# Performance work log

Measured on AMD Instinct MI355X. Metric: run time of the kernel, lower is better.

The kernel has to match this reference:

```python
import jax, jax.numpy as jnp
import numpy as np

B, N, C = 8, 4096, 512

def setup_inputs() -> dict:
    key = jax.random.key(0)
    k1, k2, k3, k4, k5, k6 = jax.random.split(key, 6)
    x = jax.random.normal(k1, (B, N, C), dtype=jnp.float32)
    adj = jax.random.uniform(k2, (B, C, C), dtype=jnp.float32)
    # params: stored [in, out] so y = x @ W + b (equivalent to torch Linear)
    s = 1.0 / np.sqrt(C)
    Wqkv = jax.random.uniform(k3, (C, 3 * C), dtype=jnp.float32, minval=-s, maxval=s)
    bqkv = jax.random.uniform(k4, (3 * C,), dtype=jnp.float32, minval=-s, maxval=s)
    Wo = jax.random.uniform(k5, (C, C), dtype=jnp.float32, minval=-s, maxval=s)
    bo = jax.random.uniform(k6, (C,), dtype=jnp.float32, minval=-s, maxval=s)
    return {"x": x, "adj": adj, "Wqkv": Wqkv, "bqkv": bqkv, "Wo": Wo, "bo": bo}

def reference(x, adj, Wqkv, bqkv, Wo, bo):
    # qkv projection + ReLU gating
    qkv = jnp.einsum('bnc,cd->bnd', x, Wqkv) + bqkv          # [B,N,3C]
    q, k, v = jnp.split(qkv, 3, axis=-1)                      # each [B,N,C]
    q, k, v = jax.nn.relu(q), jax.nn.relu(k), jax.nn.relu(v)
    dk = q.shape[-1]
    # channel-wise scores: q^T k over tokens -> [B,C,C]
    scores = jnp.einsum('bnc,bnd->bcd', q, k) / jnp.sqrt(jnp.float32(dk))
    attn = jax.nn.softmax(scores, axis=-1)
    attn = attn * adj                                         # post-softmax adjacency gate
    y = jnp.einsum('bnc,bcd->bnd', v, attn)                   # value.matmul(attention)
    return jnp.einsum('bnc,cd->bnd', y, Wo) + bo
```

## Files before the change

### kernel.cpp

```cpp
#include <hip/hip_runtime.h>

#define B_ 8
#define N_ 4096
#define C_ 512

typedef _Float16 f16;
typedef __attribute__((ext_vector_type(8))) _Float16 f16x8;
typedef __attribute__((ext_vector_type(4))) _Float16 f16x4;
typedef __attribute__((ext_vector_type(4))) float f32x4;

#define TILE_E (128 * 32)

#define GLL16(gsrc, ldst)                                                      \
  __builtin_amdgcn_global_load_lds(                                            \
      (const __attribute__((address_space(1))) void*)(gsrc),                   \
      (__attribute__((address_space(3))) void*)(ldst), 16, 0, 0)

__device__ __forceinline__ int xcd_remap(int bid, int nwg) {
  return (bid & 7) * (nwg >> 3) + (bid >> 3);
}

template <int LDA2, int LDB2, int NT>
__device__ __forceinline__ void mainloop2(const char* __restrict__ Agb,
                                          const char* __restrict__ Bgb,
                                          f16* Als, f16* Bls,
                                          f32x4 (&acc)[4][4]) {
  const int tid = threadIdx.x;
  const int lane = tid & 63;
  const int wv = tid >> 6;
  const int wr = wv >> 1;
  const int wc = wv & 1;

  const int r15 = lane & 15;
  const int kc8 = (lane >> 4) << 3;
  const int swz = (r15 & 7) << 3;
  const int k0x = kc8 ^ swz;
  const int k1x = (kc8 + 32) ^ swz;
  const int awbase = (wr * 64 + r15) * 64;
  const int bwbase = (wc * 64 + r15) * 64;

  int rowl[4], colb[4];
#pragma unroll
  for (int ld = 0; ld < 4; ++ld) {
    const int doff = (ld * 256 + tid) * 16;
    rowl[ld] = doff >> 7;
    colb[ld] = (doff & 127) ^ ((rowl[ld] & 7) << 4);
  }

  auto stage = [&](int t) {
    if (t >= NT) return;
    f16* la = Als + (t & 1) * 8192 + wv * 512;
    f16* lb = Bls + (t & 1) * 8192 + wv * 512;
#pragma unroll
    for (int ld = 0; ld < 4; ++ld) {
      GLL16(Agb + (size_t)rowl[ld] * LDA2 + (size_t)t * 128 + colb[ld],
            la + ld * 2048);
      GLL16(Bgb + (size_t)rowl[ld] * LDB2 + (size_t)t * 128 + colb[ld],
            lb + ld * 2048);
    }
  };

  stage(0);
  __syncthreads();

  for (int T = 0; T < NT; ++T) {
    stage(T + 1);
    const f16* Ab = Als + (T & 1) * 8192;
    const f16* Bb = Bls + (T & 1) * 8192;
    f16x8 af[4][2], bf[4][2];
#pragma unroll
    for (int m = 0; m < 4; ++m) {
      af[m][0] = *(const f16x8*)(Ab + awbase + m * 1024 + k0x);
      af[m][1] = *(const f16x8*)(Ab + awbase + m * 1024 + k1x);
    }
#pragma unroll
    for (int n = 0; n < 4; ++n) {
      bf[n][0] = *(const f16x8*)(Bb + bwbase + n * 1024 + k0x);
      bf[n][1] = *(const f16x8*)(Bb + bwbase + n * 1024 + k1x);
    }
#pragma unroll
    for (int s = 0; s < 2; ++s)
#pragma unroll
      for (int m = 0; m < 4; ++m)
#pragma unroll
        for (int n = 0; n < 4; ++n)
          acc[m][n] = __builtin_amdgcn_mfma_f32_16x16x32_f16(
              af[m][s], bf[n][s], acc[m][n], 0, 0, 0);
    __syncthreads();
  }
}

#define ZERO_ACC(acc)                                                          \
  f32x4 acc[4][4];                                                             \
  _Pragma("unroll") for (int zi = 0; zi < 4; ++zi)                             \
      _Pragma("unroll") for (int zj = 0; zj < 4; ++zj) {                       \
    f32x4 z = {0.f, 0.f, 0.f, 0.f};                                            \
    acc[zi][zj] = z;                                                           \
  }

__device__ __forceinline__ void run_mainloop(const f16* __restrict__ Atile,
                                             const f16* __restrict__ Btile,
                                             int lda, int ldb, int nk,
                                             f16* As, f16* Bs,
                                             f32x4 (&acc)[4][4]) {
  const int tid = threadIdx.x;
  const int lane = tid & 63;
  const int wave = tid >> 6;
  const int wr = wave >> 1, wc = wave & 1;

  auto stage = [&](int buf, int kt) {
#pragma unroll
    for (int j = 0; j < 2; ++j) {
      const int idx = j * 256 + wave * 64 + lane;
      const int row = idx >> 2;
      const int kc = idx & 3;
      GLL16(Atile + (size_t)row * lda + kt * 32 + kc * 8,
            As + buf * TILE_E + (j * 256 + wave * 64) * 8);
      GLL16(Btile + (size_t)row * ldb + kt * 32 + kc * 8,
            Bs + buf * TILE_E + (j * 256 + wave * 64) * 8);
    }
  };

  stage(0, 0);
  __syncthreads();
  for (int kt = 0; kt < nk; ++kt) {
    const int buf = kt & 1;
    if (kt + 1 < nk) stage(buf ^ 1, kt + 1);
    const f16* aB = As + buf * TILE_E;
    const f16* bB = Bs + buf * TILE_E;
    f16x8 af[4], bf[4];
#pragma unroll
    for (int i = 0; i < 4; ++i)
      af[i] = *(const f16x8*)(aB + (wr * 64 + i * 16 + (lane & 15)) * 32 +
                              ((lane >> 4) * 8));
#pragma unroll
    for (int j = 0; j < 4; ++j)
      bf[j] = *(const f16x8*)(bB + (wc * 64 + j * 16 + (lane & 15)) * 32 +
                              ((lane >> 4) * 8));
#pragma unroll
    for (int i = 0; i < 4; ++i)
#pragma unroll
      for (int j = 0; j < 4; ++j)
        acc[i][j] =
            __builtin_amdgcn_mfma_f32_16x16x32_f16(af[i], bf[j], acc[i][j],
                                                   0, 0, 0);
    __syncthreads();
  }
}

__global__ void __launch_bounds__(256) k_cvt_x(const float* __restrict__ in,
                                               f16* __restrict__ out) {
  const int i = blockIdx.x * 256 + threadIdx.x;
  float4 v = ((const float4*)in)[i];
  f16x4 h = {(f16)v.x, (f16)v.y, (f16)v.z, (f16)v.w};
  ((f16x4*)out)[i] = h;
}

__global__ void __launch_bounds__(256) k_transpose_w(const float* __restrict__ w,
                                                     f16* __restrict__ wt,
                                                     int cols) {
  const int idx = blockIdx.x * 256 + threadIdx.x;
  const int n = idx >> 9;
  const int c = idx & 511;
  wt[idx] = (f16)w[(size_t)c * cols + n];
}

__global__ void __launch_bounds__(256, 2)
    k_gemm_qkv(const f16* __restrict__ x16, const f16* __restrict__ wqkvt,
               const float* __restrict__ bqkv, f16* __restrict__ q_t,
               f16* __restrict__ k_t, f16* __restrict__ v16) {
  __shared__ alignas(16) f16 Als[2 * 8192];
  __shared__ alignas(16) f16 Bls[2 * 8192];
  const int l = xcd_remap(blockIdx.x, 3072);
  const int bx = l % 12;
  const int my = l / 12;
  const char* Agb = (const char*)(x16 + (size_t)my * 128 * C_);
  const char* Bgb = (const char*)(wqkvt + (size_t)bx * 128 * C_);
  ZERO_ACC(acc);
  mainloop2<C_ * 2, C_ * 2, C_ / 64>(Agb, Bgb, Als, Bls, acc);

  const int lane = threadIdx.x & 63, wv = threadIdx.x >> 6;
  const int wr = wv >> 1, wc = wv & 1;
  const int sec = bx >> 2;
  const int colbase = bx * 128 + wc * 64;
  const int rowbase = my * 128 + wr * 64;
  const int b = rowbase >> 12;
#pragma unroll
  for (int n = 0; n < 4; ++n) {
    const int col = colbase + n * 16 + (lane & 15);
    const int cch = col & 511;
    const float bias = bqkv[col];
#pragma unroll
    for (int m = 0; m < 4; ++m) {
      const int rg = rowbase + m * 16 + ((lane >> 4) << 2);
      const int nloc = rg & 4095;
      f32x4 a = acc[m][n];
      f16x4 h = {(f16)fmaxf(a[0] + bias, 0.f), (f16)fmaxf(a[1] + bias, 0.f),
                 (f16)fmaxf(a[2] + bias, 0.f), (f16)fmaxf(a[3] + bias, 0.f)};
      if (sec == 0) {
        *(f16x4*)(q_t + ((size_t)b * C_ + cch) * N_ + nloc) = h;
      } else if (sec == 1) {
        *(f16x4*)(k_t + ((size_t)b * C_ + cch) * N_ + nloc) = h;
      } else {
        f16* dst = v16 + (size_t)rg * C_ + cch;
        dst[0] = h[0];
        dst[C_] = h[1];
        dst[2 * C_] = h[2];
        dst[3 * C_] = h[3];
      }
    }
  }
}

__global__ void __launch_bounds__(256, 2)
    k_gemm_scores(const f16* __restrict__ q_t, const f16* __restrict__ k_t,
                  f16* __restrict__ spart) {
  __shared__ alignas(16) f16 Als[2 * 8192];
  __shared__ alignas(16) f16 Bls[2 * 8192];
  const int l = xcd_remap(blockIdx.x, 1024);
  const int bx = l & 3;
  const int by = (l >> 2) & 3;
  const int z = l >> 4;
  const int b = z >> 3, sp = z & 7;
  const char* Agb = (const char*)(q_t + (size_t)b * C_ * N_ +
                                  (size_t)(by * 128) * N_ + sp * 512);
  const char* Bgb = (const char*)(k_t + (size_t)b * C_ * N_ +
                                  (size_t)(bx * 128) * N_ + sp * 512);
  ZERO_ACC(acc);
  mainloop2<N_ * 2, N_ * 2, 8>(Agb, Bgb, Als, Bls, acc);

  const int lane = threadIdx.x & 63, wv = threadIdx.x >> 6;
  const int wr = wv >> 1, wc = wv & 1;
  f16* base = spart + (size_t)(sp * B_ + b) * C_ * C_;
#pragma unroll
  for (int n = 0; n < 4; ++n) {
    const int d = bx * 128 + wc * 64 + n * 16 + (lane & 15);
#pragma unroll
    for (int m = 0; m < 4; ++m) {
      const int c0 = by * 128 + wr * 64 + m * 16 + ((lane >> 4) << 2);
#pragma unroll
      for (int r = 0; r < 4; ++r)
        base[(size_t)(c0 + r) * C_ + d] = (f16)acc[m][n][r];
    }
  }
}

__global__ void __launch_bounds__(256)
    k_softmax_gate(const f16* __restrict__ spart,
                   const float* __restrict__ adj, f16* __restrict__ attn) {
  const int b = blockIdx.x >> 9, c = blockIdx.x & 511;
  const int tid = threadIdx.x;
  const size_t ro = ((size_t)b * C_ + c) * C_;
  float s0 = 0.f, s1 = 0.f;
#pragma unroll
  for (int sp = 0; sp < 8; ++sp) {
    const f16* p = spart + (size_t)sp * B_ * C_ * C_ + ro;
    s0 += (float)p[tid];
    s1 += (float)p[tid + 256];
  }
  const float scale = 0.044194173824159216f;
  const float v0 = s0 * scale, v1 = s1 * scale;

  __shared__ float red[256];
  red[tid] = fmaxf(v0, v1);
  __syncthreads();
  for (int s = 128; s > 0; s >>= 1) {
    if (tid < s) red[tid] = fmaxf(red[tid], red[tid + s]);
    __syncthreads();
  }
  const float mx = red[0];
  __syncthreads();
  const float e0 = __expf(v0 - mx), e1 = __expf(v1 - mx);
  red[tid] = e0 + e1;
  __syncthreads();
  for (int s = 128; s > 0; s >>= 1) {
    if (tid < s) red[tid] += red[tid + s];
    __syncthreads();
  }
  const float inv = 1.0f / red[0];
  attn[ro + tid] = (f16)(e0 * inv * adj[ro + tid]);
  attn[ro + tid + 256] = (f16)(e1 * inv * adj[ro + tid + 256]);
}

__global__ void __launch_bounds__(256)
    k_gemm_m(const f16* __restrict__ attn, const f16* __restrict__ wot,
             f16* __restrict__ mt) {
  __shared__ alignas(16) f16 As[2 * TILE_E];
  __shared__ alignas(16) f16 Bs[2 * TILE_E];
  const int b = blockIdx.z;
  const f16* Atile = attn + (size_t)b * C_ * C_ + (size_t)blockIdx.y * 128 * C_;
  const f16* Btile = wot + (size_t)blockIdx.x * 128 * C_;
  ZERO_ACC(acc);
  run_mainloop(Atile, Btile, C_, C_, C_ / 32, As, Bs, acc);

  const int tid = threadIdx.x, lane = tid & 63, wave = tid >> 6;
  const int wr = wave >> 1, wc = wave & 1;
  f16* base = mt + (size_t)b * C_ * C_;
  const int colbase = blockIdx.x * 128 + wc * 64;
  const int rowbase = blockIdx.y * 128 + wr * 64;
#pragma unroll
  for (int j = 0; j < 4; ++j) {
    const int e = colbase + j * 16 + (lane & 15);
#pragma unroll
    for (int i = 0; i < 4; ++i) {
      const int c0 = rowbase + i * 16 + ((lane >> 4) << 2);
      f32x4 a = acc[i][j];
      f16x4 h = {(f16)a[0], (f16)a[1], (f16)a[2], (f16)a[3]};
      *(f16x4*)(base + (size_t)e * C_ + c0) = h;
    }
  }
}

__global__ void __launch_bounds__(256, 2)
    k_gemm_out(const f16* __restrict__ v16, const f16* __restrict__ mt,
               const float* __restrict__ bo, float* __restrict__ out) {
  __shared__ alignas(16) f16 Als[2 * 8192];
  __shared__ alignas(16) f16 Bls[2 * 8192];
  const int l = xcd_remap(blockIdx.x, 1024);
  const int bx = l & 3;
  const int my = l >> 2;
  const int b = (my * 128) >> 12;
  const char* Agb = (const char*)(v16 + (size_t)my * 128 * C_);
  const char* Bgb = (const char*)(mt + (size_t)b * C_ * C_ +
                                  (size_t)(bx * 128) * C_);
  ZERO_ACC(acc);
  mainloop2<C_ * 2, C_ * 2, 8>(Agb, Bgb, Als, Bls, acc);

  const int lane = threadIdx.x & 63, wv = threadIdx.x >> 6;
  const int wr = wv >> 1, wc = wv & 1;
#pragma unroll
  for (int n = 0; n < 4; ++n) {
    const int e = bx * 128 + wc * 64 + n * 16 + (lane & 15);
    const float bias = bo[e];
#pragma unroll
    for (int m = 0; m < 4; ++m) {
      const int rg = my * 128 + wr * 64 + m * 16 + ((lane >> 4) << 2);
#pragma unroll
      for (int r = 0; r < 4; ++r)
        out[(size_t)(rg + r) * C_ + e] = acc[m][n][r] + bias;
    }
  }
}

extern "C" void kernel_launch(void* const* d_in, const int* in_sizes, int n_in,
                              void* d_out, int out_size, void* d_ws,
                              size_t ws_size, hipStream_t stream) {
  const float* x = (const float*)d_in[0];
  const float* adj = (const float*)d_in[1];
  const float* Wqkv = (const float*)d_in[2];
  const float* bqkv = (const float*)d_in[3];
  const float* Wo = (const float*)d_in[4];
  const float* bo = (const float*)d_in[5];
  float* out = (float*)d_out;

  char* ws = (char*)d_ws;
  size_t off = 0;
  auto carve = [&](size_t bytes) -> char* {
    char* p = ws + off;
    off += (bytes + 255) & ~(size_t)255;
    return p;
  };
  f16* x16 = (f16*)carve((size_t)B_ * N_ * C_ * 2);
  f16* wqkvt = (f16*)carve((size_t)3 * C_ * C_ * 2);
  f16* wot = (f16*)carve((size_t)C_ * C_ * 2);
  f16* q_t = (f16*)carve((size_t)B_ * C_ * N_ * 2);
  f16* k_t = (f16*)carve((size_t)B_ * C_ * N_ * 2);
  f16* v16 = (f16*)carve((size_t)B_ * N_ * C_ * 2);
  f16* spart = x16;
  f16* attn16 = k_t;
  f16* mt16 = q_t;

  k_cvt_x<<<(B_ * N_ * C_ / 4) / 256, 256, 0, stream>>>(x, x16);
  k_transpose_w<<<(C_ * 3 * C_) / 256, 256, 0, stream>>>(Wqkv, wqkvt, 3 * C_);
  k_transpose_w<<<(C_ * C_) / 256, 256, 0, stream>>>(Wo, wot, C_);
  k_gemm_qkv<<<3072, 256, 0, stream>>>(x16, wqkvt, bqkv, q_t, k_t, v16);
  k_gemm_scores<<<1024, 256, 0, stream>>>(q_t, k_t, spart);
  k_softmax_gate<<<B_ * C_, 256, 0, stream>>>(spart, adj, attn16);
  k_gemm_m<<<dim3(4, 4, B_), 256, 0, stream>>>(attn16, wot, mt16);
  k_gemm_out<<<1024, 256, 0, stream>>>(v16, mt16, bo, out);
}
```

Measured before the change: 180.0 us.

## Shrink GEMM K-tile to 32 for higher occupancy and use wave-per-row softmax

Replaces the 64-wide K-step mainloop with a 32-wide one, halving LDS per block so launch bounds can request 4 blocks per CU instead of 2. The adapted XOR swizzle is also used for the attn×Wo GEMM in place of its separate unswizzled loop. The softmax kernel is rewritten so each wavefront handles one row with vectorized loads and shuffle reductions instead of block-wide shared-memory reductions. The trade-off is twice as many K iterations and barriers per tile in exchange for more resident waves to hide latency.

```diff
diff --git a/kernel.cpp b/kernel.cpp
--- a/kernel.cpp
+++ b/kernel.cpp
@@ -9,8 +9,6 @@
 typedef __attribute__((ext_vector_type(4))) _Float16 f16x4;
 typedef __attribute__((ext_vector_type(4))) float f32x4;
 
-#define TILE_E (128 * 32)
-
 #define GLL16(gsrc, ldst)                                                      \
   __builtin_amdgcn_global_load_lds(                                            \
       (const __attribute__((address_space(1))) void*)(gsrc),                   \
@@ -21,10 +19,10 @@
 }
 
 template <int LDA2, int LDB2, int NT>
-__device__ __forceinline__ void mainloop2(const char* __restrict__ Agb,
-                                          const char* __restrict__ Bgb,
-                                          f16* Als, f16* Bls,
-                                          f32x4 (&acc)[4][4]) {
+__device__ __forceinline__ void mainloop32(const char* __restrict__ Agb,
+                                           const char* __restrict__ Bgb,
+                                           f16* Als, f16* Bls,
+                                           f32x4 (&acc)[4][4]) {
   const int tid = threadIdx.x;
   const int lane = tid & 63;
   const int wv = tid >> 6;
@@ -32,30 +30,29 @@
   const int wc = wv & 1;
 
   const int r15 = lane & 15;
-  const int kc8 = (lane >> 4) << 3;
-  const int swz = (r15 & 7) << 3;
-  const int k0x = kc8 ^ swz;
-  const int k1x = (kc8 + 32) ^ swz;
-  const int awbase = (wr * 64 + r15) * 64;
-  const int bwbase = (wc * 64 + r15) * 64;
-
-  int rowl[4], colb[4];
-#pragma unroll
-  for (int ld = 0; ld < 4; ++ld) {
+  const int g8 = (lane >> 4) << 3;
+  const int swz = (r15 & 3) << 3;
+  const int kx = g8 ^ swz;
+  const int awbase = (wr * 64 + r15) * 32;
+  const int bwbase = (wc * 64 + r15) * 32;
+
+  int rowl[2], colb[2];
+#pragma unroll
+  for (int ld = 0; ld < 2; ++ld) {
     const int doff = (ld * 256 + tid) * 16;
-    rowl[ld] = doff >> 7;
-    colb[ld] = (doff & 127) ^ ((rowl[ld] & 7) << 4);
+    rowl[ld] = doff >> 6;
+    colb[ld] = (doff & 63) ^ ((rowl[ld] & 3) << 4);
   }
 
   auto stage = [&](int t) {
     if (t >= NT) return;
-    f16* la = Als + (t & 1) * 8192 + wv * 512;
-    f16* lb = Bls + (t & 1) * 8192 + wv * 512;
-#pragma unroll
-    for (int ld = 0; ld < 4; ++ld) {
-      GLL16(Agb + (size_t)rowl[ld] * LDA2 + (size_t)t * 128 + colb[ld],
+    f16* la = Als + (t & 1) * 4096 + wv * 512;
+    f16* lb = Bls + (t & 1) * 4096 + wv * 512;
+#pragma unroll
+    for (int ld = 0; ld < 2; ++ld) {
+      GLL16(Agb + (size_t)rowl[ld] * LDA2 + (size_t)t * 64 + colb[ld],
             la + ld * 2048);
-      GLL16(Bgb + (size_t)rowl[ld] * LDB2 + (size_t)t * 128 + colb[ld],
+      GLL16(Bgb + (size_t)rowl[ld] * LDB2 + (size_t)t * 64 + colb[ld],
             lb + ld * 2048);
     }
   };
@@ -65,27 +62,21 @@
 
   for (int T = 0; T < NT; ++T) {
     stage(T + 1);
-    const f16* Ab = Als + (T & 1) * 8192;
-    const f16* Bb = Bls + (T & 1) * 8192;
-    f16x8 af[4][2], bf[4][2];
-#pragma unroll
-    for (int m = 0; m < 4; ++m) {
-      af[m][0] = *(const f16x8*)(Ab + awbase + m * 1024 + k0x);
-      af[m][1] = *(const f16x8*)(Ab + awbase + m * 1024 + k1x);
-    }
-#pragma unroll
-    for (int n = 0; n < 4; ++n) {
-      bf[n][0] = *(const f16x8*)(Bb + bwbase + n * 1024 + k0x);
-      bf[n][1] = *(const f16x8*)(Bb + bwbase + n * 1024 + k1x);
-    }
-#pragma unroll
-    for (int s = 0; s < 2; ++s)
-#pragma unroll
-      for (int m = 0; m < 4; ++m)
-#pragma unroll
-        for (int n = 0; n < 4; ++n)
-          acc[m][n] = __builtin_amdgcn_mfma_f32_16x16x32_f16(
-              af[m][s], bf[n][s], acc[m][n], 0, 0, 0);
+    const f16* Ab = Als + (T & 1) * 4096;
+    const f16* Bb = Bls + (T & 1) * 4096;
+    f16x8 af[4], bf[4];
+#pragma unroll
+    for (int m = 0; m < 4; ++m)
+      af[m] = *(const f16x8*)(Ab + awbase + m * 512 + kx);
+#pragma unroll
+    for (int n = 0; n < 4; ++n)
+      bf[n] = *(const f16x8*)(Bb + bwbase + n * 512 + kx);
+#pragma unroll
+    for (int m = 0; m < 4; ++m)
+#pragma unroll
+      for (int n = 0; n < 4; ++n)
+        acc[m][n] = __builtin_amdgcn_mfma_f32_16x16x32_f16(af[m], bf[n],
+                                                           acc[m][n], 0, 0, 0);
     __syncthreads();
   }
 }
@@ -97,56 +88,6 @@
     f32x4 z = {0.f, 0.f, 0.f, 0.f};                                            \
     acc[zi][zj] = z;                                                           \
   }
-
-__device__ __forceinline__ void run_mainloop(const f16* __restrict__ Atile,
-                                             const f16* __restrict__ Btile,
-                                             int lda, int ldb, int nk,
-                                             f16* As, f16* Bs,
-                                             f32x4 (&acc)[4][4]) {
-  const int tid = threadIdx.x;
-  const int lane = tid & 63;
-  const int wave = tid >> 6;
-  const int wr = wave >> 1, wc = wave & 1;
-
-  auto stage = [&](int buf, int kt) {
-#pragma unroll
-    for (int j = 0; j < 2; ++j) {
-      const int idx = j * 256 + wave * 64 + lane;
-      const int row = idx >> 2;
-      const int kc = idx & 3;
-      GLL16(Atile + (size_t)row * lda + kt * 32 + kc * 8,
-            As + buf * TILE_E + (j * 256 + wave * 64) * 8);
-      GLL16(Btile + (size_t)row * ldb + kt * 32 + kc * 8,
-            Bs + buf * TILE_E + (j * 256 + wave * 64) * 8);
-    }
-  };
-
-  stage(0, 0);
-  __syncthreads();
-  for (int kt = 0; kt < nk; ++kt) {
-    const int buf = kt & 1;
-    if (kt + 1 < nk) stage(buf ^ 1, kt + 1);
-    const f16* aB = As + buf * TILE_E;
-    const f16* bB = Bs + buf * TILE_E;
-    f16x8 af[4], bf[4];
-#pragma unroll
-    for (int i = 0; i < 4; ++i)
-      af[i] = *(const f16x8*)(aB + (wr * 64 + i * 16 + (lane & 15)) * 32 +
-                              ((lane >> 4) * 8));
-#pragma unroll
-    for (int j = 0; j < 4; ++j)
-      bf[j] = *(const f16x8*)(bB + (wc * 64 + j * 16 + (lane & 15)) * 32 +
-                              ((lane >> 4) * 8));
-#pragma unroll
-    for (int i = 0; i < 4; ++i)
-#pragma unroll
-      for (int j = 0; j < 4; ++j)
-        acc[i][j] =
-            __builtin_amdgcn_mfma_f32_16x16x32_f16(af[i], bf[j], acc[i][j],
-                                                   0, 0, 0);
-    __syncthreads();
-  }
-}
 
 __global__ void __launch_bounds__(256) k_cvt_x(const float* __restrict__ in,
                                                f16* __restrict__ out) {
@@ -165,19 +106,19 @@
   wt[idx] = (f16)w[(size_t)c * cols + n];
 }
 
-__global__ void __launch_bounds__(256, 2)
+__global__ void __launch_bounds__(256, 4)
     k_gemm_qkv(const f16* __restrict__ x16, const f16* __restrict__ wqkvt,
                const float* __restrict__ bqkv, f16* __restrict__ q_t,
                f16* __restrict__ k_t, f16* __restrict__ v16) {
-  __shared__ alignas(16) f16 Als[2 * 8192];
-  __shared__ alignas(16) f16 Bls[2 * 8192];
+  __shared__ alignas(16) f16 Als[2 * 4096];
+  __shared__ alignas(16) f16 Bls[2 * 4096];
   const int l = xcd_remap(blockIdx.x, 3072);
   const int bx = l % 12;
   const int my = l / 12;
   const char* Agb = (const char*)(x16 + (size_t)my * 128 * C_);
   const char* Bgb = (const char*)(wqkvt + (size_t)bx * 128 * C_);
   ZERO_ACC(acc);
-  mainloop2<C_ * 2, C_ * 2, C_ / 64>(Agb, Bgb, Als, Bls, acc);
+  mainloop32<C_ * 2, C_ * 2, C_ / 32>(Agb, Bgb, Als, Bls, acc);
 
   const int lane = threadIdx.x & 63, wv = threadIdx.x >> 6;
   const int wr = wv >> 1, wc = wv & 1;
@@ -212,11 +153,11 @@
   }
 }
 
-__global__ void __launch_bounds__(256, 2)
+__global__ void __launch_bounds__(256, 4)
     k_gemm_scores(const f16* __restrict__ q_t, const f16* __restrict__ k_t,
                   f16* __restrict__ spart) {
-  __shared__ alignas(16) f16 Als[2 * 8192];
-  __shared__ alignas(16) f16 Bls[2 * 8192];
+  __shared__ alignas(16) f16 Als[2 * 4096];
+  __shared__ alignas(16) f16 Bls[2 * 4096];
   const int l = xcd_remap(blockIdx.x, 1024);
   const int bx = l & 3;
   const int by = (l >> 2) & 3;
@@ -227,7 +168,7 @@
   const char* Bgb = (const char*)(k_t + (size_t)b * C_ * N_ +
                                   (size_t)(bx * 128) * N_ + sp * 512);
   ZERO_ACC(acc);
-  mainloop2<N_ * 2, N_ * 2, 8>(Agb, Bgb, Als, Bls, acc);
+  mainloop32<N_ * 2, N_ * 2, 16>(Agb, Bgb, Als, Bls, acc);
 
   const int lane = threadIdx.x & 63, wv = threadIdx.x >> 6;
   const int wr = wv >> 1, wc = wv & 1;
@@ -248,53 +189,60 @@
 __global__ void __launch_bounds__(256)
     k_softmax_gate(const f16* __restrict__ spart,
                    const float* __restrict__ adj, f16* __restrict__ attn) {
-  const int b = blockIdx.x >> 9, c = blockIdx.x & 511;
-  const int tid = threadIdx.x;
-  const size_t ro = ((size_t)b * C_ + c) * C_;
-  float s0 = 0.f, s1 = 0.f;
+  const int wv = threadIdx.x >> 6, lane = threadIdx.x & 63;
+  const int row = blockIdx.x * 4 + wv;
+  const size_t ro = (size_t)row * 512;
+  const int off = lane * 8;
+
+  float s[8] = {0.f, 0.f, 0.f, 0.f, 0.f, 0.f, 0.f, 0.f};
 #pragma unroll
   for (int sp = 0; sp < 8; ++sp) {
-    const f16* p = spart + (size_t)sp * B_ * C_ * C_ + ro;
-    s0 += (float)p[tid];
-    s1 += (float)p[tid + 256];
+    f16x8 v = *(const f16x8*)(spart + (size_t)sp * (B_ * C_ * C_) + ro + off);
+#pragma unroll
+    for (int i = 0; i < 8; ++i) s[i] += (float)v[i];
   }
   const float scale = 0.044194173824159216f;
-  const float v0 = s0 * scale, v1 = s1 * scale;
-
-  __shared__ float red[256];
-  red[tid] = fmaxf(v0, v1);
-  __syncthreads();
-  for (int s = 128; s > 0; s >>= 1) {
-    if (tid < s) red[tid] = fmaxf(red[tid], red[tid + s]);
-    __syncthreads();
-  }
-  const float mx = red[0];
-  __syncthreads();
-  const float e0 = __expf(v0 - mx), e1 = __expf(v1 - mx);
-  red[tid] = e0 + e1;
-  __syncthreads();
-  for (int s = 128; s > 0; s >>= 1) {
-    if (tid < s) red[tid] += red[tid + s];
-    __syncthreads();
-  }
-  const float inv = 1.0f / red[0];
-  attn[ro + tid] = (f16)(e0 * inv * adj[ro + tid]);
-  attn[ro + tid + 256] = (f16)(e1 * inv * adj[ro + tid + 256]);
+  float mx = -1e30f;
+#pragma unroll
+  for (int i = 0; i < 8; ++i) {
+    s[i] *= scale;
+    mx = fmaxf(mx, s[i]);
+  }
+#pragma unroll
+  for (int d = 32; d > 0; d >>= 1) mx = fmaxf(mx, __shfl_xor(mx, d, 64));
+  float e[8], sum = 0.f;
+#pragma unroll
+  for (int i = 0; i < 8; ++i) {
+    e[i] = __expf(s[i] - mx);
+    sum += e[i];
+  }
+#pragma unroll
+  for (int d = 32; d > 0; d >>= 1) sum += __shfl_xor(sum, d, 64);
+  const float inv = 1.0f / sum;
+  const float4 a0 = *(const float4*)(adj + ro + off);
+  const float4 a1 = *(const float4*)(adj + ro + off + 4);
+  f16x8 o;
+  o[0] = (f16)(e[0] * inv * a0.x); o[1] = (f16)(e[1] * inv * a0.y);
+  o[2] = (f16)(e[2] * inv * a0.z); o[3] = (f16)(e[3] * inv * a0.w);
+  o[4] = (f16)(e[4] * inv * a1.x); o[5] = (f16)(e[5] * inv * a1.y);
+  o[6] = (f16)(e[6] * inv * a1.z); o[7] = (f16)(e[7] * inv * a1.w);
+  *(f16x8*)(attn + ro + off) = o;
 }
 
 __global__ void __launch_bounds__(256)
     k_gemm_m(const f16* __restrict__ attn, const f16* __restrict__ wot,
              f16* __restrict__ mt) {
-  __shared__ alignas(16) f16 As[2 * TILE_E];
-  __shared__ alignas(16) f16 Bs[2 * TILE_E];
+  __shared__ alignas(16) f16 Als[2 * 4096];
+  __shared__ alignas(16) f16 Bls[2 * 4096];
   const int b = blockIdx.z;
-  const f16* Atile = attn + (size_t)b * C_ * C_ + (size_t)blockIdx.y * 128 * C_;
-  const f16* Btile = wot + (size_t)blockIdx.x * 128 * C_;
+  const char* Agb = (const char*)(attn + (size_t)b * C_ * C_ +
+                                  (size_t)blockIdx.y * 128 * C_);
+  const char* Bgb = (const char*)(wot + (size_t)blockIdx.x * 128 * C_);
   ZERO_ACC(acc);
-  run_mainloop(Atile, Btile, C_, C_, C_ / 32, As, Bs, acc);
-
-  const int tid = threadIdx.x, lane = tid & 63, wave = tid >> 6;
-  const int wr = wave >> 1, wc = wave & 1;
+  mainloop32<C_ * 2, C_ * 2, 16>(Agb, Bgb, Als, Bls, acc);
+
+  const int lane = threadIdx.x & 63, wv = threadIdx.x >> 6;
+  const int wr = wv >> 1, wc = wv & 1;
   f16* base = mt + (size_t)b * C_ * C_;
   const int colbase = blockIdx.x * 128 + wc * 64;
   const int rowbase = blockIdx.y * 128 + wr * 64;
@@ -311,11 +259,11 @@
   }
 }
 
-__global__ void __launch_bounds__(256, 2)
+__global__ void __launch_bounds__(256, 4)
     k_gemm_out(const f16* __restrict__ v16, const f16* __restrict__ mt,
                const float* __restrict__ bo, float* __restrict__ out) {
-  __shared__ alignas(16) f16 Als[2 * 8192];
-  __shared__ alignas(16) f16 Bls[2 * 8192];
+  __shared__ alignas(16) f16 Als[2 * 4096];
+  __shared__ alignas(16) f16 Bls[2 * 4096];
   const int l = xcd_remap(blockIdx.x, 1024);
   const int bx = l & 3;
   const int my = l >> 2;
@@ -324,7 +272,7 @@
   const char* Bgb = (const char*)(mt + (size_t)b * C_ * C_ +
                                   (size_t)(bx * 128) * C_);
   ZERO_ACC(acc);
-  mainloop2<C_ * 2, C_ * 2, 8>(Agb, Bgb, Als, Bls, acc);
+  mainloop32<C_ * 2, C_ * 2, 16>(Agb, Bgb, Als, Bls, acc);
 
   const int lane = threadIdx.x & 63, wv = threadIdx.x >> 6;
   const int wr = wv >> 1, wc = wv & 1;
@@ -375,7 +323,7 @@
   k_transpose_w<<<(C_ * C_) / 256, 256, 0, stream>>>(Wo, wot, C_);
   k_gemm_qkv<<<3072, 256, 0, stream>>>(x16, wqkvt, bqkv, q_t, k_t, v16);
   k_gemm_scores<<<1024, 256, 0, stream>>>(q_t, k_t, spart);
-  k_softmax_gate<<<B_ * C_, 256, 0, stream>>>(spart, adj, attn16);
+  k_softmax_gate<<<1024, 256, 0, stream>>>(spart, adj, attn16);
   k_gemm_m<<<dim3(4, 4, B_), 256, 0, stream>>>(attn16, wot, mt16);
   k_gemm_out<<<1024, 256, 0, stream>>>(v16, mt16, bo, out);
 }
```

Measured after the change: 185.7 us. 3.2% more time.
